# Kernel optimization log

Measured on AMD Instinct MI355X. Metric: run time of the kernel, lower is better.

## Reference

```python
import jax, jax.numpy as jnp
import numpy as np

N_NODES = 50000
N_EDGES = 800000
IN_DIM = 128
OUT_DIM = 64
NUM_HEADS = 4


def setup_inputs() -> dict:
    key = jax.random.key(0)
    k1, k2, k3, k4 = jax.random.split(key, 4)
    h = jax.random.normal(k1, (N_NODES, IN_DIM), dtype=jnp.float32)
    # Xavier-uniform-like init for each head's weight
    limit = float(np.sqrt(6.0 / (IN_DIM + OUT_DIM)))
    W = jax.random.uniform(k2, (NUM_HEADS, IN_DIM, OUT_DIM), dtype=jnp.float32, minval=-limit, maxval=limit)
    b = jnp.zeros((OUT_DIM,), dtype=jnp.float32)
    src = jax.random.randint(k3, (N_EDGES,), 0, N_NODES, dtype=jnp.int32)
    dst = jax.random.randint(k4, (N_EDGES,), 0, N_NODES, dtype=jnp.int32)
    return {"h": h, "W": W, "b": b, "src": src, "dst": dst}


def reference(h, W, b, src, dst):
    # Multi-head projection averaged over heads: (1/K) * sum_k h @ W_k  -> [N, out_dim]
    hp = jnp.einsum('nd,kdf->nf', h, W) / W.shape[0]
    # copy_src + sum aggregation: scatter-sum messages h[src] into dst nodes
    msgs = hp[src]  # [E, out_dim]
    agg = jax.ops.segment_sum(msgs, dst, num_segments=h.shape[0])  # [N, out_dim]
    return jax.nn.relu(agg + b)
```

## Files before the change

kernel.cpp:

```cpp
#include <hip/hip_runtime.h>

#define N_NODES 50000
#define N_EDGES 800000
#define IN_DIM 128
#define OUT_DIM 64
#define PAD 64
#define NPART 6250
#define FCHUNK 2048
#define NCHUNK ((N_EDGES + FCHUNK - 1) / FCHUNK)
#define WAVG_BLOCKS 32

typedef __attribute__((ext_vector_type(8))) short bf16x8;
typedef __attribute__((ext_vector_type(4))) float f32x4;

__device__ inline unsigned short f2bf(float x) {
    unsigned u = __builtin_bit_cast(unsigned, x);
    unsigned r = (u + 0x7FFFu + ((u >> 16) & 1u)) >> 16;
    return (unsigned short)r;
}

__global__ __launch_bounds__(256) void wf_kernel(const float* __restrict__ W,
                                                 unsigned short* __restrict__ wT,
                                                 const int* __restrict__ src,
                                                 const int* __restrict__ dst,
                                                 int* __restrict__ cnt,
                                                 unsigned short* __restrict__ esrc) {
    if (blockIdx.x < WAVG_BLOCKS) {
        const int i = blockIdx.x * 256 + threadIdx.x;
        const int f = i >> 7, d = i & 127;
        float s = W[d * 64 + f] + W[8192 + d * 64 + f] +
                  W[16384 + d * 64 + f] + W[24576 + d * 64 + f];
        wT[i] = f2bf(0.25f * s);
        return;
    }
    const int bb = blockIdx.x - WAVG_BLOCKS;
    const int p = bb & 7;
    const int chunk = bb >> 3;
    const int e0 = chunk * FCHUNK;
    for (int e = e0 + threadIdx.x; e < e0 + FCHUNK && e < N_EDGES; e += 256) {
        const int d = dst[e];
        const int s = src[e];
        if (d / NPART == p) {
            int pos = atomicAdd(&cnt[d], 1);
            if (pos < PAD) esrc[(size_t)d * PAD + pos] = (unsigned short)s;
        }
    }
}

__global__ __launch_bounds__(256) void gemm_mfma_kernel(const float* __restrict__ h,
                                                        const unsigned short* __restrict__ wT,
                                                        unsigned short* __restrict__ hp) {
    const int wave = (blockIdx.x << 2) + (threadIdx.x >> 6);
    const int n0 = wave << 4;
    if (n0 >= N_NODES) return;
    const int lane = threadIdx.x & 63;
    const int lm = lane & 15;
    const int lg = lane >> 4;

    bf16x8 bfrag[4][4];
#pragma unroll
    for (int nt = 0; nt < 4; ++nt)
#pragma unroll
        for (int ks = 0; ks < 4; ++ks)
            bfrag[nt][ks] = *(const bf16x8*)&wT[(nt * 16 + lm) * 128 + ks * 32 + lg * 8];

    f32x4 acc[4];
#pragma unroll
    for (int nt = 0; nt < 4; ++nt) acc[nt] = (f32x4)0.0f;

    const float* hrow = h + (size_t)(n0 + lm) * IN_DIM;
#pragma unroll
    for (int ks = 0; ks < 4; ++ks) {
        const float4 a0 = *(const float4*)&hrow[ks * 32 + lg * 8];
        const float4 a1 = *(const float4*)&hrow[ks * 32 + lg * 8 + 4];
        bf16x8 af;
        af[0] = (short)f2bf(a0.x); af[1] = (short)f2bf(a0.y);
        af[2] = (short)f2bf(a0.z); af[3] = (short)f2bf(a0.w);
        af[4] = (short)f2bf(a1.x); af[5] = (short)f2bf(a1.y);
        af[6] = (short)f2bf(a1.z); af[7] = (short)f2bf(a1.w);
#pragma unroll
        for (int nt = 0; nt < 4; ++nt)
            acc[nt] = __builtin_amdgcn_mfma_f32_16x16x32_bf16(af, bfrag[nt][ks], acc[nt], 0, 0, 0);
    }

#pragma unroll
    for (int nt = 0; nt < 4; ++nt)
#pragma unroll
        for (int r = 0; r < 4; ++r) {
            const int m = lg * 4 + r;
            hp[(size_t)(n0 + m) * 64 + nt * 16 + lm] = f2bf(acc[nt][r]);
        }
}

__global__ __launch_bounds__(256) void gather_kernel(const unsigned short* __restrict__ hp,
                                                     const unsigned short* __restrict__ esrc,
                                                     const int* __restrict__ cnt,
                                                     const float* __restrict__ bias,
                                                     float* __restrict__ out) {
    const int n = blockIdx.x * 16 + (threadIdx.x >> 4);
    const int l = threadIdx.x & 15;
    if (n >= N_NODES) return;

    int deg = cnt[n];
    deg = deg > PAD ? PAD : deg;

    const uint2 sv = ((const uint2*)(esrc + (size_t)n * PAD))[l];
    const uint2* hp2 = (const uint2*)hp;

    float a0 = 0.f, a1 = 0.f, a2 = 0.f, a3 = 0.f;

    for (int j0 = 0; j0 < deg; j0 += 16) {
        const int m = deg - j0;
        const int b = j0 >> 2;
        uint2 v[16];
#pragma unroll
        for (int k = 0; k < 16; ++k) {
            unsigned w = __shfl(((k >> 1) & 1) ? sv.y : sv.x, b + (k >> 2), 16);
            unsigned sid = (k & 1) ? (w >> 16) : (w & 0xFFFFu);
            v[k] = hp2[(size_t)sid * 16 + l];
        }
        __builtin_amdgcn_sched_barrier(0);
#pragma unroll
        for (int k = 0; k < 16; ++k) {
            if (k < m) {
                a0 += __builtin_bit_cast(float, v[k].x << 16);
                a1 += __builtin_bit_cast(float, v[k].x & 0xFFFF0000u);
                a2 += __builtin_bit_cast(float, v[k].y << 16);
                a3 += __builtin_bit_cast(float, v[k].y & 0xFFFF0000u);
            }
        }
    }

    const float4 bv = ((const float4*)bias)[l];
    float4 o;
    o.x = fmaxf(a0 + bv.x, 0.f);
    o.y = fmaxf(a1 + bv.y, 0.f);
    o.z = fmaxf(a2 + bv.z, 0.f);
    o.w = fmaxf(a3 + bv.w, 0.f);
    ((float4*)out)[(size_t)n * 16 + l] = o;
}

extern "C" void kernel_launch(void* const* d_in, const int* in_sizes, int n_in,
                              void* d_out, int out_size, void* d_ws, size_t ws_size,
                              hipStream_t stream) {
    const float* h   = (const float*)d_in[0];
    const float* W   = (const float*)d_in[1];
    const float* b   = (const float*)d_in[2];
    const int*   src = (const int*)d_in[3];
    const int*   dst = (const int*)d_in[4];
    float* out = (float*)d_out;

    char* p = (char*)d_ws;
    unsigned short* wT = (unsigned short*)p;          p += 32 * 1024;
    unsigned short* hp = (unsigned short*)p;          p += (size_t)N_NODES * OUT_DIM * 2;
    int* cnt = (int*)p;                               p += (size_t)N_NODES * 4;
    unsigned short* esrc = (unsigned short*)p;

    hipMemsetAsync(cnt, 0, (size_t)N_NODES * 4, stream);

    wf_kernel<<<WAVG_BLOCKS + NCHUNK * 8, 256, 0, stream>>>(W, wT, src, dst, cnt, esrc);
    gemm_mfma_kernel<<<(N_NODES / 16 + 3) / 4, 256, 0, stream>>>(h, wT, hp);
    gather_kernel<<<(N_NODES + 15) / 16, 256, 0, stream>>>(hp, esrc, cnt, b, out);
}
```

Baseline: 145.6 us.

## Bind edge-fill partitions to XCC ids and split gather into feature halves

The fill kernel now reads the hardware XCC id and uses it to pick which destination partition a block handles. Blocks then pull edge chunks from a per-XCC atomic work cursor, so the atomics and esrc writes for one partition stay on a single XCC's L2. The projected features are stored as two 32-column halves, and gather runs twice, once per half, so each pass's random-access working set (3.2 MB) is smaller and more cache-resident. The costs are an extra kernel launch, reading esrc and cnt twice, and reliance on hardware XCC numbering with a dynamic cursor scheme.

```diff
diff --git a/kernel.cpp b/kernel.cpp
--- a/kernel.cpp
+++ b/kernel.cpp
@@ -9,6 +9,7 @@
 #define FCHUNK 2048
 #define NCHUNK ((N_EDGES + FCHUNK - 1) / FCHUNK)
 #define WAVG_BLOCKS 32
+#define FILL_BLOCKS 2048
 
 typedef __attribute__((ext_vector_type(8))) short bf16x8;
 typedef __attribute__((ext_vector_type(4))) float f32x4;
@@ -24,6 +25,7 @@
                                                  const int* __restrict__ src,
                                                  const int* __restrict__ dst,
                                                  int* __restrict__ cnt,
+                                                 int* __restrict__ cursor8,
                                                  unsigned short* __restrict__ esrc) {
     if (blockIdx.x < WAVG_BLOCKS) {
         const int i = blockIdx.x * 256 + threadIdx.x;
@@ -33,23 +35,37 @@
         wT[i] = f2bf(0.25f * s);
         return;
     }
-    const int bb = blockIdx.x - WAVG_BLOCKS;
-    const int p = bb & 7;
-    const int chunk = bb >> 3;
-    const int e0 = chunk * FCHUNK;
-    for (int e = e0 + threadIdx.x; e < e0 + FCHUNK && e < N_EDGES; e += 256) {
-        const int d = dst[e];
-        const int s = src[e];
-        if (d / NPART == p) {
-            int pos = atomicAdd(&cnt[d], 1);
-            if (pos < PAD) esrc[(size_t)d * PAD + pos] = (unsigned short)s;
+
+    int xcc;
+    asm volatile("s_getreg_b32 %0, hwreg(20)" : "=s"(xcc));
+    xcc &= 7;
+    const int lo = xcc * NPART;
+    const int hi = lo + NPART;
+
+    __shared__ int s_chunk;
+    for (;;) {
+        if (threadIdx.x == 0) s_chunk = atomicAdd(&cursor8[xcc], 1);
+        __syncthreads();
+        const int chunk = s_chunk;
+        __syncthreads();
+        if (chunk >= NCHUNK) break;
+        const int e0 = chunk * FCHUNK;
+        const int e1 = (e0 + FCHUNK < N_EDGES) ? e0 + FCHUNK : N_EDGES;
+        for (int e = e0 + (int)threadIdx.x; e < e1; e += 256) {
+            const int d = dst[e];
+            const int s = src[e];
+            if (d >= lo && d < hi) {
+                int pos = atomicAdd(&cnt[d], 1);
+                if (pos < PAD) esrc[(size_t)d * PAD + pos] = (unsigned short)s;
+            }
         }
     }
 }
 
 __global__ __launch_bounds__(256) void gemm_mfma_kernel(const float* __restrict__ h,
                                                         const unsigned short* __restrict__ wT,
-                                                        unsigned short* __restrict__ hp) {
+                                                        unsigned short* __restrict__ hp0,
+                                                        unsigned short* __restrict__ hp1) {
     const int wave = (blockIdx.x << 2) + (threadIdx.x >> 6);
     const int n0 = wave << 4;
     if (n0 >= N_NODES) return;
@@ -88,15 +104,18 @@
 #pragma unroll
         for (int r = 0; r < 4; ++r) {
             const int m = lg * 4 + r;
-            hp[(size_t)(n0 + m) * 64 + nt * 16 + lm] = f2bf(acc[nt][r]);
+            unsigned short val = f2bf(acc[nt][r]);
+            if (nt < 2) hp0[(size_t)(n0 + m) * 32 + nt * 16 + lm] = val;
+            else        hp1[(size_t)(n0 + m) * 32 + (nt - 2) * 16 + lm] = val;
         }
 }
 
-__global__ __launch_bounds__(256) void gather_kernel(const unsigned short* __restrict__ hp,
+__global__ __launch_bounds__(256) void gather_kernel(const unsigned* __restrict__ hph,
                                                      const unsigned short* __restrict__ esrc,
                                                      const int* __restrict__ cnt,
                                                      const float* __restrict__ bias,
-                                                     float* __restrict__ out) {
+                                                     float* __restrict__ out,
+                                                     int half) {
     const int n = blockIdx.x * 16 + (threadIdx.x >> 4);
     const int l = threadIdx.x & 15;
     if (n >= N_NODES) return;
@@ -105,39 +124,34 @@
     deg = deg > PAD ? PAD : deg;
 
     const uint2 sv = ((const uint2*)(esrc + (size_t)n * PAD))[l];
-    const uint2* hp2 = (const uint2*)hp;
 
-    float a0 = 0.f, a1 = 0.f, a2 = 0.f, a3 = 0.f;
+    float a0 = 0.f, a1 = 0.f;
 
     for (int j0 = 0; j0 < deg; j0 += 16) {
         const int m = deg - j0;
         const int b = j0 >> 2;
-        uint2 v[16];
+        unsigned v[16];
 #pragma unroll
         for (int k = 0; k < 16; ++k) {
             unsigned w = __shfl(((k >> 1) & 1) ? sv.y : sv.x, b + (k >> 2), 16);
             unsigned sid = (k & 1) ? (w >> 16) : (w & 0xFFFFu);
-            v[k] = hp2[(size_t)sid * 16 + l];
+            v[k] = hph[((size_t)sid << 4) + l];
         }
         __builtin_amdgcn_sched_barrier(0);
 #pragma unroll
         for (int k = 0; k < 16; ++k) {
             if (k < m) {
-                a0 += __builtin_bit_cast(float, v[k].x << 16);
-                a1 += __builtin_bit_cast(float, v[k].x & 0xFFFF0000u);
-                a2 += __builtin_bit_cast(float, v[k].y << 16);
-                a3 += __builtin_bit_cast(float, v[k].y & 0xFFFF0000u);
+                a0 += __builtin_bit_cast(float, v[k] << 16);
+                a1 += __builtin_bit_cast(float, v[k] & 0xFFFF0000u);
             }
         }
     }
 
-    const float4 bv = ((const float4*)bias)[l];
-    float4 o;
+    const float2 bv = ((const float2*)bias)[(half << 4) + l];
+    float2 o;
     o.x = fmaxf(a0 + bv.x, 0.f);
     o.y = fmaxf(a1 + bv.y, 0.f);
-    o.z = fmaxf(a2 + bv.z, 0.f);
-    o.w = fmaxf(a3 + bv.w, 0.f);
-    ((float4*)out)[(size_t)n * 16 + l] = o;
+    ((float2*)out)[(size_t)n * 32 + (half << 4) + l] = o;
 }
 
 extern "C" void kernel_launch(void* const* d_in, const int* in_sizes, int n_in,
@@ -151,14 +165,17 @@
     float* out = (float*)d_out;
 
     char* p = (char*)d_ws;
-    unsigned short* wT = (unsigned short*)p;          p += 32 * 1024;
-    unsigned short* hp = (unsigned short*)p;          p += (size_t)N_NODES * OUT_DIM * 2;
-    int* cnt = (int*)p;                               p += (size_t)N_NODES * 4;
+    unsigned short* wT  = (unsigned short*)p;   p += 32 * 1024;
+    unsigned short* hp0 = (unsigned short*)p;   p += (size_t)N_NODES * 32 * 2;
+    unsigned short* hp1 = (unsigned short*)p;   p += (size_t)N_NODES * 32 * 2;
+    int* cnt = (int*)p;                         p += (size_t)(N_NODES + 8) * 4;
+    int* cursor8 = cnt + N_NODES;
     unsigned short* esrc = (unsigned short*)p;
 
-    hipMemsetAsync(cnt, 0, (size_t)N_NODES * 4, stream);
+    hipMemsetAsync(cnt, 0, (size_t)(N_NODES + 8) * 4, stream);
 
-    wf_kernel<<<WAVG_BLOCKS + NCHUNK * 8, 256, 0, stream>>>(W, wT, src, dst, cnt, esrc);
-    gemm_mfma_kernel<<<(N_NODES / 16 + 3) / 4, 256, 0, stream>>>(h, wT, hp);
-    gather_kernel<<<(N_NODES + 15) / 16, 256, 0, stream>>>(hp, esrc, cnt, b, out);
+    wf_kernel<<<WAVG_BLOCKS + FILL_BLOCKS, 256, 0, stream>>>(W, wT, src, dst, cnt, cursor8, esrc);
+    gemm_mfma_kernel<<<(N_NODES / 16 + 3) / 4, 256, 0, stream>>>(h, wT, hp0, hp1);
+    gather_kernel<<<(N_NODES + 15) / 16, 256, 0, stream>>>((const unsigned*)hp0, esrc, cnt, b, out, 0);
+    gather_kernel<<<(N_NODES + 15) / 16, 256, 0, stream>>>((const unsigned*)hp1, esrc, cnt, b, out, 1);
 }
```

Measured after the change: 191.0 us. +31.2%, slower.

## Fuse all stages into one cooperative persistent kernel with binned edge bucketing

Applied to the files above, without the earlier changes.

Replaces the memset plus three kernel launches with a single cooperative kernel that uses grid-wide syncs between phases. Edge bucketing now runs in two passes: a per-chunk shared-memory histogram into 196 coarse dst bins with packed (local dst, src) entries in scratch, then a per-bin pass that builds per-node padded source lists in shared memory and writes them out coalesced. This removes the 8x redundant scan of the edge arrays and the global per-node atomics. It also overlaps the bucketing with the projection GEMM in the same phase. In exchange it adds grid syncs, a larger scratch buffer, and an overflow cap of 5120 entries per bin.

```diff
diff --git a/kernel.cpp b/kernel.cpp
--- a/kernel.cpp
+++ b/kernel.cpp
@@ -1,14 +1,19 @@
 #include <hip/hip_runtime.h>
+#include <hip/hip_cooperative_groups.h>
 
 #define N_NODES 50000
 #define N_EDGES 800000
 #define IN_DIM 128
 #define OUT_DIM 64
 #define PAD 64
-#define NPART 6250
+#define BINS 196
+#define BCAP 5120
 #define FCHUNK 2048
-#define NCHUNK ((N_EDGES + FCHUNK - 1) / FCHUNK)
-#define WAVG_BLOCKS 32
+#define NCHUNK 391
+#define WAVG_VB 32
+#define GEMM_VB 782
+#define GATH_VB 3125
+#define MAX_GRID 1024
 
 typedef __attribute__((ext_vector_type(8))) short bf16x8;
 typedef __attribute__((ext_vector_type(4))) float f32x4;
@@ -19,125 +24,167 @@
     return (unsigned short)r;
 }
 
-__global__ __launch_bounds__(256) void wf_kernel(const float* __restrict__ W,
-                                                 unsigned short* __restrict__ wT,
-                                                 const int* __restrict__ src,
-                                                 const int* __restrict__ dst,
-                                                 int* __restrict__ cnt,
-                                                 unsigned short* __restrict__ esrc) {
-    if (blockIdx.x < WAVG_BLOCKS) {
-        const int i = blockIdx.x * 256 + threadIdx.x;
+__global__ __launch_bounds__(256, 4) void mega_kernel(
+    const float* __restrict__ h, const float* __restrict__ W,
+    const float* __restrict__ bias, const int* __restrict__ src,
+    const int* __restrict__ dst, float* __restrict__ out,
+    unsigned short* __restrict__ wT, unsigned short* __restrict__ hp,
+    int* __restrict__ cnt, int* __restrict__ binCursor,
+    unsigned short* __restrict__ esrc, unsigned* __restrict__ scratch)
+{
+    __shared__ __align__(16) unsigned char smem[32 * 1024 + 1024 + 816];
+    cooperative_groups::grid_group grid = cooperative_groups::this_grid();
+    const int t = threadIdx.x;
+
+    for (unsigned vb = blockIdx.x; vb < WAVG_VB; vb += gridDim.x) {
+        const int i = (int)vb * 256 + t;
         const int f = i >> 7, d = i & 127;
         float s = W[d * 64 + f] + W[8192 + d * 64 + f] +
                   W[16384 + d * 64 + f] + W[24576 + d * 64 + f];
         wT[i] = f2bf(0.25f * s);
-        return;
-    }
-    const int bb = blockIdx.x - WAVG_BLOCKS;
-    const int p = bb & 7;
-    const int chunk = bb >> 3;
-    const int e0 = chunk * FCHUNK;
-    for (int e = e0 + threadIdx.x; e < e0 + FCHUNK && e < N_EDGES; e += 256) {
-        const int d = dst[e];
-        const int s = src[e];
-        if (d / NPART == p) {
-            int pos = atomicAdd(&cnt[d], 1);
-            if (pos < PAD) esrc[(size_t)d * PAD + pos] = (unsigned short)s;
+    }
+    if (blockIdx.x == gridDim.x - 1 && t < BINS) binCursor[t] = 0;
+    grid.sync();
+
+    for (unsigned vb = blockIdx.x; vb < GEMM_VB + NCHUNK; vb += gridDim.x) {
+        if (vb < GEMM_VB) {
+            const int wave = ((int)vb << 2) + (t >> 6);
+            const int n0 = wave << 4;
+            if (n0 < N_NODES) {
+                const int lane = t & 63;
+                const int lm = lane & 15;
+                const int lg = lane >> 4;
+
+                bf16x8 bfrag[4][4];
+#pragma unroll
+                for (int nt = 0; nt < 4; ++nt)
+#pragma unroll
+                    for (int ks = 0; ks < 4; ++ks)
+                        bfrag[nt][ks] = *(const bf16x8*)&wT[(nt * 16 + lm) * 128 + ks * 32 + lg * 8];
+
+                f32x4 acc[4];
+#pragma unroll
+                for (int nt = 0; nt < 4; ++nt) acc[nt] = (f32x4)0.0f;
+
+                const float* hrow = h + (size_t)(n0 + lm) * IN_DIM;
+#pragma unroll
+                for (int ks = 0; ks < 4; ++ks) {
+                    const float4 a0 = *(const float4*)&hrow[ks * 32 + lg * 8];
+                    const float4 a1 = *(const float4*)&hrow[ks * 32 + lg * 8 + 4];
+                    bf16x8 af;
+                    af[0] = (short)f2bf(a0.x); af[1] = (short)f2bf(a0.y);
+                    af[2] = (short)f2bf(a0.z); af[3] = (short)f2bf(a0.w);
+                    af[4] = (short)f2bf(a1.x); af[5] = (short)f2bf(a1.y);
+                    af[6] = (short)f2bf(a1.z); af[7] = (short)f2bf(a1.w);
+#pragma unroll
+                    for (int nt = 0; nt < 4; ++nt)
+                        acc[nt] = __builtin_amdgcn_mfma_f32_16x16x32_bf16(af, bfrag[nt][ks], acc[nt], 0, 0, 0);
+                }
+#pragma unroll
+                for (int nt = 0; nt < 4; ++nt)
+#pragma unroll
+                    for (int r = 0; r < 4; ++r) {
+                        const int m = lg * 4 + r;
+                        hp[(size_t)(n0 + m) * 64 + nt * 16 + lm] = f2bf(acc[nt][r]);
+                    }
+            }
+        } else {
+            const int blk = (int)vb - GEMM_VB;
+            int* hist = (int*)smem;
+            int* base = hist + BINS;
+            const int e0 = blk * FCHUNK;
+            const int e1 = (e0 + FCHUNK < N_EDGES) ? e0 + FCHUNK : N_EDGES;
+
+            for (int i = t; i < BINS; i += 256) hist[i] = 0;
+            __syncthreads();
+            for (int e = e0 + t; e < e1; e += 256)
+                atomicAdd(&hist[dst[e] >> 8], 1);
+            __syncthreads();
+            for (int i = t; i < BINS; i += 256)
+                base[i] = atomicAdd(&binCursor[i], hist[i]);
+            __syncthreads();
+            for (int e = e0 + t; e < e1; e += 256) {
+                const int d = dst[e];
+                const int bin = d >> 8;
+                const int pos = atomicAdd(&base[bin], 1);
+                if (pos < BCAP)
+                    scratch[(size_t)bin * BCAP + pos] =
+                        ((unsigned)(d & 255) << 16) | (unsigned)src[e];
+            }
+            __syncthreads();
         }
     }
-}
-
-__global__ __launch_bounds__(256) void gemm_mfma_kernel(const float* __restrict__ h,
-                                                        const unsigned short* __restrict__ wT,
-                                                        unsigned short* __restrict__ hp) {
-    const int wave = (blockIdx.x << 2) + (threadIdx.x >> 6);
-    const int n0 = wave << 4;
-    if (n0 >= N_NODES) return;
-    const int lane = threadIdx.x & 63;
-    const int lm = lane & 15;
-    const int lg = lane >> 4;
-
-    bf16x8 bfrag[4][4];
-#pragma unroll
-    for (int nt = 0; nt < 4; ++nt)
-#pragma unroll
-        for (int ks = 0; ks < 4; ++ks)
-            bfrag[nt][ks] = *(const bf16x8*)&wT[(nt * 16 + lm) * 128 + ks * 32 + lg * 8];
-
-    f32x4 acc[4];
-#pragma unroll
-    for (int nt = 0; nt < 4; ++nt) acc[nt] = (f32x4)0.0f;
-
-    const float* hrow = h + (size_t)(n0 + lm) * IN_DIM;
-#pragma unroll
-    for (int ks = 0; ks < 4; ++ks) {
-        const float4 a0 = *(const float4*)&hrow[ks * 32 + lg * 8];
-        const float4 a1 = *(const float4*)&hrow[ks * 32 + lg * 8 + 4];
-        bf16x8 af;
-        af[0] = (short)f2bf(a0.x); af[1] = (short)f2bf(a0.y);
-        af[2] = (short)f2bf(a0.z); af[3] = (short)f2bf(a0.w);
-        af[4] = (short)f2bf(a1.x); af[5] = (short)f2bf(a1.y);
-        af[6] = (short)f2bf(a1.z); af[7] = (short)f2bf(a1.w);
-#pragma unroll
-        for (int nt = 0; nt < 4; ++nt)
-            acc[nt] = __builtin_amdgcn_mfma_f32_16x16x32_bf16(af, bfrag[nt][ks], acc[nt], 0, 0, 0);
-    }
-
-#pragma unroll
-    for (int nt = 0; nt < 4; ++nt)
-#pragma unroll
-        for (int r = 0; r < 4; ++r) {
-            const int m = lg * 4 + r;
-            hp[(size_t)(n0 + m) * 64 + nt * 16 + lm] = f2bf(acc[nt][r]);
+    grid.sync();
+
+    for (unsigned vb = blockIdx.x; vb < BINS; vb += gridDim.x) {
+        unsigned short* buck = (unsigned short*)smem;
+        int* lcnt = (int*)(smem + 32 * 1024);
+        lcnt[t] = 0;
+        __syncthreads();
+
+        int ne = binCursor[vb];
+        if (ne > BCAP) ne = BCAP;
+        const unsigned* sp = scratch + (size_t)vb * BCAP;
+        for (int i = t; i < ne; i += 256) {
+            const unsigned pk = sp[i];
+            const int dl = pk >> 16;
+            const int pos = atomicAdd(&lcnt[dl], 1);
+            if (pos < PAD) buck[dl * PAD + pos] = (unsigned short)(pk & 0xFFFFu);
         }
-}
-
-__global__ __launch_bounds__(256) void gather_kernel(const unsigned short* __restrict__ hp,
-                                                     const unsigned short* __restrict__ esrc,
-                                                     const int* __restrict__ cnt,
-                                                     const float* __restrict__ bias,
-                                                     float* __restrict__ out) {
-    const int n = blockIdx.x * 16 + (threadIdx.x >> 4);
-    const int l = threadIdx.x & 15;
-    if (n >= N_NODES) return;
-
-    int deg = cnt[n];
-    deg = deg > PAD ? PAD : deg;
-
-    const uint2 sv = ((const uint2*)(esrc + (size_t)n * PAD))[l];
+        __syncthreads();
+
+        const int n0 = (int)vb << 8;
+        if (n0 + t < N_NODES) cnt[n0 + t] = lcnt[t];
+        int nvalid = N_NODES - n0;
+        if (nvalid > 256) nvalid = 256;
+        uint4* eg = (uint4*)(esrc + (size_t)n0 * PAD);
+        const uint4* bl = (const uint4*)buck;
+        for (int i = t; i < nvalid * 8; i += 256) eg[i] = bl[i];
+        __syncthreads();
+    }
+    grid.sync();
+
     const uint2* hp2 = (const uint2*)hp;
-
-    float a0 = 0.f, a1 = 0.f, a2 = 0.f, a3 = 0.f;
-
-    for (int j0 = 0; j0 < deg; j0 += 16) {
-        const int m = deg - j0;
-        const int b = j0 >> 2;
-        uint2 v[16];
-#pragma unroll
-        for (int k = 0; k < 16; ++k) {
-            unsigned w = __shfl(((k >> 1) & 1) ? sv.y : sv.x, b + (k >> 2), 16);
-            unsigned sid = (k & 1) ? (w >> 16) : (w & 0xFFFFu);
-            v[k] = hp2[(size_t)sid * 16 + l];
+    for (unsigned vb = blockIdx.x; vb < GATH_VB; vb += gridDim.x) {
+        const int n = (int)vb * 16 + (t >> 4);
+        const int l = t & 15;
+
+        int deg = cnt[n];
+        deg = deg > PAD ? PAD : deg;
+
+        const uint2 sv = ((const uint2*)(esrc + (size_t)n * PAD))[l];
+
+        float a0 = 0.f, a1 = 0.f, a2 = 0.f, a3 = 0.f;
+        for (int j0 = 0; j0 < deg; j0 += 16) {
+            const int m = deg - j0;
+            const int b = j0 >> 2;
+            uint2 v[16];
+#pragma unroll
+            for (int k = 0; k < 16; ++k) {
+                unsigned w = __shfl(((k >> 1) & 1) ? sv.y : sv.x, b + (k >> 2), 16);
+                unsigned sid = (k & 1) ? (w >> 16) : (w & 0xFFFFu);
+                v[k] = hp2[((size_t)sid << 4) + l];
+            }
+            __builtin_amdgcn_sched_barrier(0);
+#pragma unroll
+            for (int k = 0; k < 16; ++k) {
+                if (k < m) {
+                    a0 += __builtin_bit_cast(float, v[k].x << 16);
+                    a1 += __builtin_bit_cast(float, v[k].x & 0xFFFF0000u);
+                    a2 += __builtin_bit_cast(float, v[k].y << 16);
+                    a3 += __builtin_bit_cast(float, v[k].y & 0xFFFF0000u);
+                }
+            }
         }
-        __builtin_amdgcn_sched_barrier(0);
-#pragma unroll
-        for (int k = 0; k < 16; ++k) {
-            if (k < m) {
-                a0 += __builtin_bit_cast(float, v[k].x << 16);
-                a1 += __builtin_bit_cast(float, v[k].x & 0xFFFF0000u);
-                a2 += __builtin_bit_cast(float, v[k].y << 16);
-                a3 += __builtin_bit_cast(float, v[k].y & 0xFFFF0000u);
-            }
-        }
-    }
-
-    const float4 bv = ((const float4*)bias)[l];
-    float4 o;
-    o.x = fmaxf(a0 + bv.x, 0.f);
-    o.y = fmaxf(a1 + bv.y, 0.f);
-    o.z = fmaxf(a2 + bv.z, 0.f);
-    o.w = fmaxf(a3 + bv.w, 0.f);
-    ((float4*)out)[(size_t)n * 16 + l] = o;
+
+        const float4 bv = ((const float4*)bias)[l];
+        float4 o;
+        o.x = fmaxf(a0 + bv.x, 0.f);
+        o.y = fmaxf(a1 + bv.y, 0.f);
+        o.z = fmaxf(a2 + bv.z, 0.f);
+        o.w = fmaxf(a3 + bv.w, 0.f);
+        ((float4*)out)[(size_t)n * 16 + l] = o;
+    }
 }
 
 extern "C" void kernel_launch(void* const* d_in, const int* in_sizes, int n_in,
@@ -151,14 +198,22 @@
     float* out = (float*)d_out;
 
     char* p = (char*)d_ws;
-    unsigned short* wT = (unsigned short*)p;          p += 32 * 1024;
-    unsigned short* hp = (unsigned short*)p;          p += (size_t)N_NODES * OUT_DIM * 2;
-    int* cnt = (int*)p;                               p += (size_t)N_NODES * 4;
-    unsigned short* esrc = (unsigned short*)p;
-
-    hipMemsetAsync(cnt, 0, (size_t)N_NODES * 4, stream);
-
-    wf_kernel<<<WAVG_BLOCKS + NCHUNK * 8, 256, 0, stream>>>(W, wT, src, dst, cnt, esrc);
-    gemm_mfma_kernel<<<(N_NODES / 16 + 3) / 4, 256, 0, stream>>>(h, wT, hp);
-    gather_kernel<<<(N_NODES + 15) / 16, 256, 0, stream>>>(hp, esrc, cnt, b, out);
+    unsigned short* wT  = (unsigned short*)p;   p += 32 * 1024;
+    unsigned short* hp  = (unsigned short*)p;   p += (size_t)N_NODES * OUT_DIM * 2;
+    int* cnt = (int*)p;                         p += (size_t)N_NODES * 4;
+    int* binCursor = (int*)p;                   p += 1024;
+    unsigned short* esrc = (unsigned short*)p;  p += (size_t)N_NODES * PAD * 2;
+    unsigned* scratch = (unsigned*)p;
+
+    int nb = 0;
+    hipOccupancyMaxActiveBlocksPerMultiprocessor(&nb, mega_kernel, 256, 0);
+    if (nb < 1) nb = 1;
+    int gridBlocks = nb * 256;
+    if (gridBlocks > MAX_GRID) gridBlocks = MAX_GRID;
+
+    void* args[] = {(void*)&h, (void*)&W, (void*)&b, (void*)&src, (void*)&dst,
+                    (void*)&out, (void*)&wT, (void*)&hp, (void*)&cnt,
+                    (void*)&binCursor, (void*)&esrc, (void*)&scratch};
+    hipLaunchCooperativeKernel((void*)mega_kernel, dim3(gridBlocks), dim3(256),
+                               args, 0, stream);
 }
```

Result: slower. 301.4 us (+107.1%).
